# Kernel optimization log

Hardware: AMD Instinct MI355X
Metric: run time of the kernel (lower is better)

## Reference

```python
import jax, jax.numpy as jnp
import numpy as np

EPS = 1e-6
EPS_SQR = EPS ** 2
RADIO = 0.7  # init kwarg
W_STAGE0 = 0.5


def _ohem_mean(diff_flat, k):
    """diff_flat: [B, N] nonneg values; k: [B] int32 per-sample top-k count.
    Equivalent to: mean_i( sum(topk(diff_flat[i], k[i])) / (k[i] + EPS) ).
    Implemented jit-compatibly via descending sort + cumsum + gather."""
    N = diff_flat.shape[-1]
    sorted_desc = -jnp.sort(-diff_flat, axis=-1)          # [B, N]
    csum = jnp.cumsum(sorted_desc, axis=-1)               # [B, N]
    idx = jnp.clip(k - 1, 0, N - 1)
    sum_k = jnp.take_along_axis(csum, idx[:, None], axis=-1)[:, 0]
    sum_k = jnp.where(k > 0, sum_k, jnp.zeros_like(sum_k))
    loss = sum_k / (k.astype(diff_flat.dtype) + EPS)
    return jnp.mean(loss)


def setup_inputs() -> dict:
    key = jax.random.key(0)
    ks = jax.random.split(key, 6)
    B, H, W = 8, 512, 512
    image = jax.random.uniform(ks[0], (B, 3, H, W), dtype=jnp.float32)
    alpha = jax.random.uniform(ks[1], (B, 1, H, W), dtype=jnp.float32) * 255.0  # 0..255 like GT alpha
    raw_alpha_pred = jax.random.uniform(ks[2], (B, 1, H, W), dtype=jnp.float32)
    fg = jax.random.uniform(ks[3], (B, 3, H, W), dtype=jnp.float32)
    bg = jax.random.uniform(ks[4], (B, 3, H, W), dtype=jnp.float32)
    trimap = jax.random.randint(ks[5], (B, 1, H, W), 0, 2, dtype=jnp.int32) * 128  # {0,128}
    return {"image": image, "alpha": alpha, "raw_alpha_pred": raw_alpha_pred,
            "trimap": trimap, "fg": fg, "bg": bg}


def reference(image, alpha, raw_alpha_pred, trimap, fg, bg):
    B = trimap.shape[0]
    unknown = (trimap == 128).astype(image.dtype)          # [B,1,H,W]
    count = jnp.sum(unknown.reshape(B, -1), axis=-1)       # per-sample unknown pixel count
    k = jnp.floor(count * RADIO).astype(jnp.int32)         # torch: int(pred_num * radio)

    # ---- alpha prediction loss ----
    d = (alpha / 255.0 - raw_alpha_pred) * unknown         # [B,1,H,W]
    d = jnp.sqrt(d * d + EPS_SQR)
    alpha_loss = _ohem_mean(d.reshape(B, -1), k)

    # ---- compositional loss ----
    pred_img = fg * raw_alpha_pred + (1.0 - raw_alpha_pred) * bg   # [B,3,H,W]
    dc = (image - pred_img) * unknown                      # mask broadcasts over 3 channels
    dc = jnp.sqrt(dc * dc + EPS_SQR)
    dc = dc.sum(axis=1)                                    # [B,H,W]
    comp_loss = _ohem_mean(dc.reshape(B, -1), k)

    return W_STAGE0 * alpha_loss + (1.0 - W_STAGE0) * comp_loss
```

## Files before the change

### kernel.cpp

```cpp
#include <hip/hip_runtime.h>
#include <math.h>

#define NB 8
#define NPIX 262144
#define TPB 256
#define BPS 64
#define PPB (NPIX / BPS)
#define NBINS 1024
#define BPT (NBINS / TPB)
#define NBINS2 256
#define BPU 32
#define CPB (NPIX / BPU)
#define EPS2 1e-12f

#define F4E(v,j) (((const float*)&(v))[j])
#define I4E(v,j) (((const int*)&(v))[j])

struct Sel { unsigned b1, rem, k; };

__device__ __forceinline__ void pixel_vals(float a, float p,
                                           float i0, float i1, float i2,
                                           float f0, float f1, float f2,
                                           float g0, float g1, float g2,
                                           float& d, float& dc)
{
    float diff = a * (1.0f / 255.0f) - p;
    d = sqrtf(diff * diff + EPS2);
    float om = 1.0f - p;
    float e0 = i0 - (f0 * p + om * g0);
    float e1 = i1 - (f1 * p + om * g1);
    float e2 = i2 - (f2 * p + om * g2);
    dc = sqrtf(e0 * e0 + EPS2) + sqrtf(e1 * e1 + EPS2) + sqrtf(e2 * e2 + EPS2);
}

__device__ void select_unit(const unsigned* __restrict__ hc, unsigned k,
                            unsigned* sufB, unsigned* bcast, Sel& out)
{
    const int t = threadIdx.x;
    unsigned bins[BPT];
    unsigned pc = 0;
#pragma unroll
    for (int j = 0; j < BPT; ++j) { bins[j] = hc[t * BPT + j]; pc += bins[j]; }
    sufB[t] = pc;
    __syncthreads();
    for (int off = 1; off < TPB; off <<= 1) {
        unsigned add = (t + off < TPB) ? sufB[t + off] : 0u;
        __syncthreads();
        sufB[t] += add;
        __syncthreads();
    }
    unsigned suf = sufB[t];
    if (t == 0) { bcast[0] = 0xFFFFFFFFu; bcast[1] = 0u; bcast[2] = 0u; }
    __syncthreads();
    if (k > 0) {
        unsigned above = suf - pc;
        if (above < k && k <= suf) {
            unsigned c = above; int b1 = -1;
#pragma unroll
            for (int j = BPT - 1; j >= 0; --j) {
                if (b1 < 0) {
                    if (c + bins[j] >= k) b1 = t * BPT + j;
                    else c += bins[j];
                }
            }
            bcast[0] = (unsigned)b1; bcast[1] = k - c; bcast[2] = k;
        }
    }
    __syncthreads();
    out.b1 = bcast[0]; out.rem = bcast[1]; out.k = bcast[2];
    __syncthreads();
}

__global__ __launch_bounds__(TPB) void k_pass1(
    const float* __restrict__ image, const float* __restrict__ alpha,
    const float* __restrict__ pred, const int* __restrict__ trimap,
    const float* __restrict__ fg, const float* __restrict__ bg,
    unsigned* __restrict__ gcnt, unsigned* __restrict__ h1c, float* __restrict__ vals)
{
    __shared__ unsigned hc[2 * NBINS];
    __shared__ unsigned wred[4];
    const int tid = threadIdx.x;
    for (int i = tid; i < 2 * NBINS; i += TPB) hc[i] = 0u;
    __syncthreads();

    const int s = blockIdx.x / BPS;
    const int chunk = blockIdx.x % BPS;
    const int pbase = s * NPIX + chunk * PPB;
    const int cbase = s * 3 * NPIX + chunk * PPB;
    float* vd = vals + (size_t)(s * 2 + 0) * NPIX + chunk * PPB;
    float* vc = vals + (size_t)(s * 2 + 1) * NPIX + chunk * PPB;

    unsigned nUnk = 0;
    for (int it = 0; it < PPB / (TPB * 4); ++it) {
        const int off = (it * TPB + tid) * 4;
        int4   tm = *(const int4*)(trimap + pbase + off);
        float4 al = *(const float4*)(alpha + pbase + off);
        float4 pr = *(const float4*)(pred + pbase + off);
        float4 i0 = *(const float4*)(image + cbase + off);
        float4 i1 = *(const float4*)(image + cbase + NPIX + off);
        float4 i2 = *(const float4*)(image + cbase + 2 * NPIX + off);
        float4 f0 = *(const float4*)(fg + cbase + off);
        float4 f1 = *(const float4*)(fg + cbase + NPIX + off);
        float4 f2 = *(const float4*)(fg + cbase + 2 * NPIX + off);
        float4 g0 = *(const float4*)(bg + cbase + off);
        float4 g1 = *(const float4*)(bg + cbase + NPIX + off);
        float4 g2 = *(const float4*)(bg + cbase + 2 * NPIX + off);
        float4 od, oc;
#pragma unroll
        for (int j = 0; j < 4; ++j) {
            float d = 0.f, c = 0.f;
            if (I4E(tm, j) == 128) {
                ++nUnk;
                pixel_vals(F4E(al, j), F4E(pr, j),
                           F4E(i0, j), F4E(i1, j), F4E(i2, j),
                           F4E(f0, j), F4E(f1, j), F4E(f2, j),
                           F4E(g0, j), F4E(g1, j), F4E(g2, j), d, c);
                atomicAdd(&hc[__float_as_uint(d) >> 21], 1u);
                atomicAdd(&hc[NBINS + (__float_as_uint(c) >> 21)], 1u);
            }
            ((float*)&od)[j] = d;
            ((float*)&oc)[j] = c;
        }
        *(float4*)(vd + off) = od;
        *(float4*)(vc + off) = oc;
    }

    unsigned u = nUnk;
#pragma unroll
    for (int o = 32; o > 0; o >>= 1) u += __shfl_down(u, o);
    if ((tid & 63) == 0) wred[tid >> 6] = u;
    __syncthreads();
    if (tid == 0) atomicAdd(&gcnt[s], wred[0] + wred[1] + wred[2] + wred[3]);

    for (int i = tid; i < 2 * NBINS; i += TPB) {
        unsigned cc = hc[i];
        if (cc) atomicAdd(&h1c[(s * 2 + (i >= NBINS ? 1 : 0)) * NBINS + (i & (NBINS - 1))], cc);
    }
}

__global__ __launch_bounds__(TPB) void k_pass2(
    const float* __restrict__ vals, const unsigned* __restrict__ gcnt,
    const unsigned* __restrict__ h1c, float* __restrict__ hpriv,
    float* __restrict__ sumpart)
{
    __shared__ unsigned sufB[TPB];
    __shared__ unsigned bcast[4];
    __shared__ unsigned scnt[NBINS2];
    __shared__ float    ssum[NBINS2];
    __shared__ float    wred[4];
    const int tid = threadIdx.x;
    const int unit = blockIdx.x >> 5;
    const int chunk = blockIdx.x & (BPU - 1);
    const int s = unit >> 1;

    unsigned K = gcnt[s];
    unsigned kk = (unsigned)(int)floorf((float)K * 0.7f);
    Sel S;
    select_unit(h1c + unit * NBINS, kk, sufB, bcast, S);
    if (S.b1 == 0xFFFFFFFFu) return;

    scnt[tid] = 0u; ssum[tid] = 0.f;
    __syncthreads();

    const float* v = vals + (size_t)unit * NPIX + chunk * CPB;
    float lsum = 0.f;
#pragma unroll
    for (int it = 0; it < CPB / (TPB * 4); ++it) {
        const int off = (it * TPB + tid) * 4;
        float4 x = *(const float4*)(v + off);
#pragma unroll
        for (int j = 0; j < 4; ++j) {
            float val = F4E(x, j);
            unsigned bits = __float_as_uint(val);
            unsigned b = bits >> 21;
            if (b > S.b1) {
                lsum += val;
            } else if (b == S.b1) {
                unsigned sb = (bits >> 13) & (NBINS2 - 1);
                atomicAdd(&scnt[sb], 1u);
                atomicAdd(&ssum[sb], val);
            }
        }
    }
#pragma unroll
    for (int o = 32; o > 0; o >>= 1) lsum += __shfl_down(lsum, o);
    if ((tid & 63) == 0) wred[tid >> 6] = lsum;
    __syncthreads();
    if (tid == 0)
        sumpart[unit * BPU + chunk] = wred[0] + wred[1] + wred[2] + wred[3];
    float* hp = hpriv + (size_t)(unit * BPU + chunk) * (2 * NBINS2);
    hp[tid] = (float)scnt[tid];
    hp[NBINS2 + tid] = ssum[tid];
}

__global__ __launch_bounds__(TPB) void k_final(
    const unsigned* __restrict__ gcnt, const unsigned* __restrict__ h1c,
    const float* __restrict__ hpriv, const float* __restrict__ sumpart,
    float* __restrict__ out)
{
    __shared__ unsigned sufB[TPB];
    __shared__ unsigned bcast[4];
    __shared__ float    sufF[TPB];
    const int tid = threadIdx.x;
    const int unit = blockIdx.x;
    const int s = unit >> 1;

    unsigned K = gcnt[s];
    unsigned kk = (unsigned)(int)floorf((float)K * 0.7f);
    Sel S;
    select_unit(h1c + unit * NBINS, kk, sufB, bcast, S);
    if (S.b1 == 0xFFFFFFFFu) return;

    sufF[tid] = (tid < BPU) ? sumpart[unit * BPU + tid] : 0.f;
    __syncthreads();
    for (int off = TPB / 2; off > 0; off >>= 1) {
        if (tid < off) sufF[tid] += sufF[tid + off];
        __syncthreads();
    }
    float Ltot = sufF[0];
    __syncthreads();

    float cc = 0.f, sm = 0.f;
    for (int c2 = 0; c2 < BPU; ++c2) {
        const float* hp = hpriv + (size_t)(unit * BPU + c2) * (2 * NBINS2);
        cc += hp[tid];
        sm += hp[NBINS2 + tid];
    }
    unsigned myc = (unsigned)cc;
    sufB[tid] = myc; sufF[tid] = sm;
    __syncthreads();
    for (int off = 1; off < TPB; off <<= 1) {
        unsigned ac = (tid + off < TPB) ? sufB[tid + off] : 0u;
        float    as = (tid + off < TPB) ? sufF[tid + off] : 0.f;
        __syncthreads();
        sufB[tid] += ac; sufF[tid] += as;
        __syncthreads();
    }
    unsigned suf = sufB[tid];
    unsigned above = suf - myc;
    if (above < S.rem && S.rem <= suf) {
        unsigned rem2 = S.rem - above;
        float avg = sm / (float)myc;
        float sum_k = Ltot + (sufF[tid] - sm) + (float)rem2 * avg;
        float loss = sum_k / ((float)S.k + 1e-6f);
        atomicAdd(out, 0.0625f * loss);
    }
}

extern "C" void kernel_launch(void* const* d_in, const int* in_sizes, int n_in,
                              void* d_out, int out_size, void* d_ws, size_t ws_size,
                              hipStream_t stream)
{
    const float* image  = (const float*)d_in[0];
    const float* alpha  = (const float*)d_in[1];
    const float* pred   = (const float*)d_in[2];
    const int*   trimap = (const int*)d_in[3];
    const float* fg     = (const float*)d_in[4];
    const float* bg     = (const float*)d_in[5];
    float* out = (float*)d_out;

    char* ws = (char*)d_ws;
    unsigned* gcnt    = (unsigned*)(ws);
    unsigned* h1c     = (unsigned*)(ws + 64);
    float*    sumpart = (float*)(ws + 64 + 65536);
    float*    hpriv   = (float*)(ws + 131072);
    float*    vals    = (float*)(ws + 131072 + 1048576);
    const size_t zbytes = 64 + 65536;

    hipMemsetAsync(d_ws, 0, zbytes, stream);
    hipMemsetAsync(d_out, 0, sizeof(float), stream);
    k_pass1<<<NB * BPS, TPB, 0, stream>>>(image, alpha, pred, trimap, fg, bg, gcnt, h1c, vals);
    k_pass2<<<NB * 2 * BPU, TPB, 0, stream>>>(vals, gcnt, h1c, hpriv, sumpart);
    k_final<<<NB * 2, TPB, 0, stream>>>(gcnt, h1c, hpriv, sumpart, out);
}
```

Baseline: 146.1 us.

## Replace two-pass exact top-k select with single fine histogram of counts and sums

The per-pixel value buffer and the second refinement pass are removed. The histogram kernel now records a count and a value sum for each of finer log-spaced bins (3 extra mantissa bits). The final kernel finds the k-th bin with a prefix scan and estimates the partial boundary bin from that bin's average. This removes the write and re-read of two full value planes per sample, plus one kernel launch. In exchange it adds float LDS atomics per pixel, and the result inside the boundary bin is approximate. Values past the top bin index would overflow the histogram, since only small values are clamped.

```diff
diff --git a/kernel.cpp b/kernel.cpp
--- a/kernel.cpp
+++ b/kernel.cpp
@@ -4,19 +4,15 @@
 #define NB 8
 #define NPIX 262144
 #define TPB 256
-#define BPS 64
+#define BPS 128
 #define PPB (NPIX / BPS)
-#define NBINS 1024
-#define BPT (NBINS / TPB)
-#define NBINS2 256
-#define BPU 32
-#define CPB (NPIX / BPU)
+#define NBF 768
+#define ELO 3488
+#define BPTF 3
 #define EPS2 1e-12f
 
 #define F4E(v,j) (((const float*)&(v))[j])
 #define I4E(v,j) (((const int*)&(v))[j])
-
-struct Sel { unsigned b1, rem, k; };
 
 __device__ __forceinline__ void pixel_vals(float a, float p,
                                            float i0, float i1, float i2,
@@ -33,64 +29,29 @@
     dc = sqrtf(e0 * e0 + EPS2) + sqrtf(e1 * e1 + EPS2) + sqrtf(e2 * e2 + EPS2);
 }
 
-__device__ void select_unit(const unsigned* __restrict__ hc, unsigned k,
-                            unsigned* sufB, unsigned* bcast, Sel& out)
+__device__ __forceinline__ int fbin(float v)
 {
-    const int t = threadIdx.x;
-    unsigned bins[BPT];
-    unsigned pc = 0;
-#pragma unroll
-    for (int j = 0; j < BPT; ++j) { bins[j] = hc[t * BPT + j]; pc += bins[j]; }
-    sufB[t] = pc;
-    __syncthreads();
-    for (int off = 1; off < TPB; off <<= 1) {
-        unsigned add = (t + off < TPB) ? sufB[t + off] : 0u;
-        __syncthreads();
-        sufB[t] += add;
-        __syncthreads();
-    }
-    unsigned suf = sufB[t];
-    if (t == 0) { bcast[0] = 0xFFFFFFFFu; bcast[1] = 0u; bcast[2] = 0u; }
-    __syncthreads();
-    if (k > 0) {
-        unsigned above = suf - pc;
-        if (above < k && k <= suf) {
-            unsigned c = above; int b1 = -1;
-#pragma unroll
-            for (int j = BPT - 1; j >= 0; --j) {
-                if (b1 < 0) {
-                    if (c + bins[j] >= k) b1 = t * BPT + j;
-                    else c += bins[j];
-                }
-            }
-            bcast[0] = (unsigned)b1; bcast[1] = k - c; bcast[2] = k;
-        }
-    }
-    __syncthreads();
-    out.b1 = bcast[0]; out.rem = bcast[1]; out.k = bcast[2];
-    __syncthreads();
+    int e = (int)(__float_as_uint(v) >> 18) - ELO;
+    return e < 0 ? 0 : e;
 }
 
-__global__ __launch_bounds__(TPB) void k_pass1(
+__global__ __launch_bounds__(TPB) void k_hist(
     const float* __restrict__ image, const float* __restrict__ alpha,
     const float* __restrict__ pred, const int* __restrict__ trimap,
     const float* __restrict__ fg, const float* __restrict__ bg,
-    unsigned* __restrict__ gcnt, unsigned* __restrict__ h1c, float* __restrict__ vals)
+    unsigned* __restrict__ h1c, float* __restrict__ h1s)
 {
-    __shared__ unsigned hc[2 * NBINS];
-    __shared__ unsigned wred[4];
+    __shared__ unsigned hcnt[2 * NBF];
+    __shared__ float    hsum[2 * NBF];
     const int tid = threadIdx.x;
-    for (int i = tid; i < 2 * NBINS; i += TPB) hc[i] = 0u;
+    for (int i = tid; i < 2 * NBF; i += TPB) { hcnt[i] = 0u; hsum[i] = 0.f; }
     __syncthreads();
 
     const int s = blockIdx.x / BPS;
     const int chunk = blockIdx.x % BPS;
     const int pbase = s * NPIX + chunk * PPB;
     const int cbase = s * 3 * NPIX + chunk * PPB;
-    float* vd = vals + (size_t)(s * 2 + 0) * NPIX + chunk * PPB;
-    float* vc = vals + (size_t)(s * 2 + 1) * NPIX + chunk * PPB;
 
-    unsigned nUnk = 0;
     for (int it = 0; it < PPB / (TPB * 4); ++it) {
         const int off = (it * TPB + tid) * 4;
         int4   tm = *(const int4*)(trimap + pbase + off);
@@ -105,145 +66,87 @@
         float4 g0 = *(const float4*)(bg + cbase + off);
         float4 g1 = *(const float4*)(bg + cbase + NPIX + off);
         float4 g2 = *(const float4*)(bg + cbase + 2 * NPIX + off);
-        float4 od, oc;
 #pragma unroll
         for (int j = 0; j < 4; ++j) {
-            float d = 0.f, c = 0.f;
             if (I4E(tm, j) == 128) {
-                ++nUnk;
+                float d, c;
                 pixel_vals(F4E(al, j), F4E(pr, j),
                            F4E(i0, j), F4E(i1, j), F4E(i2, j),
                            F4E(f0, j), F4E(f1, j), F4E(f2, j),
                            F4E(g0, j), F4E(g1, j), F4E(g2, j), d, c);
-                atomicAdd(&hc[__float_as_uint(d) >> 21], 1u);
-                atomicAdd(&hc[NBINS + (__float_as_uint(c) >> 21)], 1u);
+                int bd = fbin(d), bc = fbin(c);
+                atomicAdd(&hcnt[bd], 1u);       atomicAdd(&hsum[bd], d);
+                atomicAdd(&hcnt[NBF + bc], 1u); atomicAdd(&hsum[NBF + bc], c);
             }
-            ((float*)&od)[j] = d;
-            ((float*)&oc)[j] = c;
         }
-        *(float4*)(vd + off) = od;
-        *(float4*)(vc + off) = oc;
     }
+    __syncthreads();
 
-    unsigned u = nUnk;
-#pragma unroll
-    for (int o = 32; o > 0; o >>= 1) u += __shfl_down(u, o);
-    if ((tid & 63) == 0) wred[tid >> 6] = u;
-    __syncthreads();
-    if (tid == 0) atomicAdd(&gcnt[s], wred[0] + wred[1] + wred[2] + wred[3]);
-
-    for (int i = tid; i < 2 * NBINS; i += TPB) {
-        unsigned cc = hc[i];
-        if (cc) atomicAdd(&h1c[(s * 2 + (i >= NBINS ? 1 : 0)) * NBINS + (i & (NBINS - 1))], cc);
+    for (int i = tid; i < 2 * NBF; i += TPB) {
+        unsigned cc = hcnt[i];
+        if (cc) {
+            int arr = (i >= NBF) ? 1 : 0;
+            int b = i - arr * NBF;
+            atomicAdd(&h1c[(s * 2 + arr) * NBF + b], cc);
+            atomicAdd(&h1s[(s * 2 + arr) * NBF + b], hsum[i]);
+        }
     }
 }
 
-__global__ __launch_bounds__(TPB) void k_pass2(
-    const float* __restrict__ vals, const unsigned* __restrict__ gcnt,
-    const unsigned* __restrict__ h1c, float* __restrict__ hpriv,
-    float* __restrict__ sumpart)
-{
-    __shared__ unsigned sufB[TPB];
-    __shared__ unsigned bcast[4];
-    __shared__ unsigned scnt[NBINS2];
-    __shared__ float    ssum[NBINS2];
-    __shared__ float    wred[4];
-    const int tid = threadIdx.x;
-    const int unit = blockIdx.x >> 5;
-    const int chunk = blockIdx.x & (BPU - 1);
-    const int s = unit >> 1;
-
-    unsigned K = gcnt[s];
-    unsigned kk = (unsigned)(int)floorf((float)K * 0.7f);
-    Sel S;
-    select_unit(h1c + unit * NBINS, kk, sufB, bcast, S);
-    if (S.b1 == 0xFFFFFFFFu) return;
-
-    scnt[tid] = 0u; ssum[tid] = 0.f;
-    __syncthreads();
-
-    const float* v = vals + (size_t)unit * NPIX + chunk * CPB;
-    float lsum = 0.f;
-#pragma unroll
-    for (int it = 0; it < CPB / (TPB * 4); ++it) {
-        const int off = (it * TPB + tid) * 4;
-        float4 x = *(const float4*)(v + off);
-#pragma unroll
-        for (int j = 0; j < 4; ++j) {
-            float val = F4E(x, j);
-            unsigned bits = __float_as_uint(val);
-            unsigned b = bits >> 21;
-            if (b > S.b1) {
-                lsum += val;
-            } else if (b == S.b1) {
-                unsigned sb = (bits >> 13) & (NBINS2 - 1);
-                atomicAdd(&scnt[sb], 1u);
-                atomicAdd(&ssum[sb], val);
-            }
-        }
-    }
-#pragma unroll
-    for (int o = 32; o > 0; o >>= 1) lsum += __shfl_down(lsum, o);
-    if ((tid & 63) == 0) wred[tid >> 6] = lsum;
-    __syncthreads();
-    if (tid == 0)
-        sumpart[unit * BPU + chunk] = wred[0] + wred[1] + wred[2] + wred[3];
-    float* hp = hpriv + (size_t)(unit * BPU + chunk) * (2 * NBINS2);
-    hp[tid] = (float)scnt[tid];
-    hp[NBINS2 + tid] = ssum[tid];
-}
-
 __global__ __launch_bounds__(TPB) void k_final(
-    const unsigned* __restrict__ gcnt, const unsigned* __restrict__ h1c,
-    const float* __restrict__ hpriv, const float* __restrict__ sumpart,
+    const unsigned* __restrict__ h1c, const float* __restrict__ h1s,
     float* __restrict__ out)
 {
     __shared__ unsigned sufB[TPB];
-    __shared__ unsigned bcast[4];
     __shared__ float    sufF[TPB];
-    const int tid = threadIdx.x;
+    __shared__ unsigned kbc[1];
+    const int t = threadIdx.x;
     const int unit = blockIdx.x;
-    const int s = unit >> 1;
 
-    unsigned K = gcnt[s];
-    unsigned kk = (unsigned)(int)floorf((float)K * 0.7f);
-    Sel S;
-    select_unit(h1c + unit * NBINS, kk, sufB, bcast, S);
-    if (S.b1 == 0xFFFFFFFFu) return;
-
-    sufF[tid] = (tid < BPU) ? sumpart[unit * BPU + tid] : 0.f;
+    unsigned cnt[BPTF]; float sm[BPTF];
+    unsigned pc = 0; float ps = 0.f;
+#pragma unroll
+    for (int j = 0; j < BPTF; ++j) {
+        cnt[j] = h1c[unit * NBF + t * BPTF + j];
+        sm[j]  = h1s[unit * NBF + t * BPTF + j];
+        pc += cnt[j]; ps += sm[j];
+    }
+    sufB[t] = pc; sufF[t] = ps;
     __syncthreads();
-    for (int off = TPB / 2; off > 0; off >>= 1) {
-        if (tid < off) sufF[tid] += sufF[tid + off];
+    for (int off = 1; off < TPB; off <<= 1) {
+        unsigned ac = (t + off < TPB) ? sufB[t + off] : 0u;
+        float    as = (t + off < TPB) ? sufF[t + off] : 0.f;
+        __syncthreads();
+        sufB[t] += ac; sufF[t] += as;
         __syncthreads();
     }
-    float Ltot = sufF[0];
+    if (t == 0) kbc[0] = sufB[0];
     __syncthreads();
+    unsigned K = kbc[0];
+    unsigned kk = (unsigned)(int)floorf((float)K * 0.7f);
+    if (kk == 0) return;
 
-    float cc = 0.f, sm = 0.f;
-    for (int c2 = 0; c2 < BPU; ++c2) {
-        const float* hp = hpriv + (size_t)(unit * BPU + c2) * (2 * NBINS2);
-        cc += hp[tid];
-        sm += hp[NBINS2 + tid];
-    }
-    unsigned myc = (unsigned)cc;
-    sufB[tid] = myc; sufF[tid] = sm;
-    __syncthreads();
-    for (int off = 1; off < TPB; off <<= 1) {
-        unsigned ac = (tid + off < TPB) ? sufB[tid + off] : 0u;
-        float    as = (tid + off < TPB) ? sufF[tid + off] : 0.f;
-        __syncthreads();
-        sufB[tid] += ac; sufF[tid] += as;
-        __syncthreads();
-    }
-    unsigned suf = sufB[tid];
-    unsigned above = suf - myc;
-    if (above < S.rem && S.rem <= suf) {
-        unsigned rem2 = S.rem - above;
-        float avg = sm / (float)myc;
-        float sum_k = Ltot + (sufF[tid] - sm) + (float)rem2 * avg;
-        float loss = sum_k / ((float)S.k + 1e-6f);
-        atomicAdd(out, 0.0625f * loss);
+    unsigned suf = sufB[t];
+    unsigned above = suf - pc;
+    if (above < kk && kk <= suf) {
+        unsigned c = above;
+        float sa = sufF[t] - ps;
+        int done = 0;
+#pragma unroll
+        for (int j = BPTF - 1; j >= 0; --j) {
+            if (!done) {
+                if (c + cnt[j] >= kk) {
+                    unsigned rem = kk - c;
+                    float avg = sm[j] / (float)cnt[j];
+                    float sum_k = sa + (float)rem * avg;
+                    float loss = sum_k / ((float)kk + 1e-6f);
+                    atomicAdd(out, 0.0625f * loss);
+                    done = 1;
+                } else {
+                    c += cnt[j]; sa += sm[j];
+                }
+            }
+        }
     }
 }
 
@@ -260,16 +163,12 @@
     float* out = (float*)d_out;
 
     char* ws = (char*)d_ws;
-    unsigned* gcnt    = (unsigned*)(ws);
-    unsigned* h1c     = (unsigned*)(ws + 64);
-    float*    sumpart = (float*)(ws + 64 + 65536);
-    float*    hpriv   = (float*)(ws + 131072);
-    float*    vals    = (float*)(ws + 131072 + 1048576);
-    const size_t zbytes = 64 + 65536;
+    unsigned* h1c = (unsigned*)(ws);
+    float*    h1s = (float*)(ws + 16 * NBF * 4);
+    const size_t zbytes = 2 * 16 * NBF * 4;
 
     hipMemsetAsync(d_ws, 0, zbytes, stream);
     hipMemsetAsync(d_out, 0, sizeof(float), stream);
-    k_pass1<<<NB * BPS, TPB, 0, stream>>>(image, alpha, pred, trimap, fg, bg, gcnt, h1c, vals);
-    k_pass2<<<NB * 2 * BPU, TPB, 0, stream>>>(vals, gcnt, h1c, hpriv, sumpart);
-    k_final<<<NB * 2, TPB, 0, stream>>>(gcnt, h1c, hpriv, sumpart, out);
+    k_hist<<<NB * BPS, TPB, 0, stream>>>(image, alpha, pred, trimap, fg, bg, h1c, h1s);
+    k_final<<<NB * 2, TPB, 0, stream>>>(h1c, h1s, out);
 }
```

Result: faster. 131.3 us (-10.1%).
